# Optimization experiments

Measured on AMD Instinct MI355X. Metric: run time of the kernel, lower is better.

The kernel has to match this reference:

```python
import jax, jax.numpy as jnp
import numpy as np

D_MODEL, D_K, D_V, H, GRID = 512, 64, 64, 8, 196
B = 4


def setup_inputs() -> dict:
    key = jax.random.key(0)
    ks = jax.random.split(key, 12)
    s = 0.02
    return {
        "queries": jax.random.normal(ks[0], (B, GRID, D_MODEL), jnp.float32),
        "keys": jax.random.normal(ks[1], (B, GRID, D_MODEL), jnp.float32),
        "values": jax.random.normal(ks[2], (B, GRID, D_MODEL), jnp.float32),
        "Wq": jax.random.normal(ks[3], (H * D_K, D_MODEL), jnp.float32) * s,
        "bq": jnp.zeros((H * D_K,), jnp.float32),
        "Wk": jax.random.normal(ks[4], (H * D_K, D_MODEL), jnp.float32) * s,
        "bk": jnp.zeros((H * D_K,), jnp.float32),
        "Wv": jax.random.normal(ks[5], (H * D_V, D_MODEL), jnp.float32) * s,
        "bv": jnp.zeros((H * D_V,), jnp.float32),
        "Wo": jax.random.normal(ks[6], (D_MODEL, H * D_V), jnp.float32) * s,
        "bo": jnp.zeros((D_MODEL,), jnp.float32),
        "scale": jnp.ones((1, H, GRID, GRID), jnp.float32) / np.sqrt(D_K).astype(np.float32),
    }


def reference(queries, keys, values, Wq, bq, Wk, bk, Wv, bv, Wo, bo, scale):
    b, nq, _ = queries.shape
    nk = values.shape[1]
    # linear projections (torch nn.Linear: x @ W.T + b)
    q_sig = queries @ Wq.T + bq          # (b, nq, h*dk)
    k_p = keys @ Wk.T + bk               # (b, nk, h*dk)
    v_p = values @ Wv.T + bv             # (b, nk, h*dv)
    # elementwise q*k interaction (b, nq, nk, h*dk)
    att_e = q_sig[:, :, None, :] * k_p[:, None, :, :]
    # sigmoid-gated values
    v_g = jax.nn.sigmoid(att_e) * v_p[:, None, :, :]
    v = v_g.reshape(b, nq, nk, H, D_K).transpose(0, 3, 1, 2, 4)      # (b,h,nq,nk,dk)
    att = att_e.reshape(b, nq, nk, H, D_K).transpose(0, 3, 1, 2, 4)  # (b,h,nq,nk,dk)
    att = att.sum(-1) * scale            # (b,h,nq,nk)
    p = jax.nn.softmax(att, axis=-1)     # dropout is identity in eval mode
    # (att.unsqueeze(-2) @ v).squeeze(-2)
    image = jnp.einsum("bhqk,bhqkd->bhqd", p, v)
    image = image.transpose(0, 2, 1, 3).reshape(b, nq, H * D_V)
    out = image @ Wo.T + bo              # (b, nq, d_model)
    out = jax.nn.sigmoid(q_sig * out) * out
    return out
```

## Files before the change

kernel.cpp:

```cpp
#include <hip/hip_runtime.h>
#include <hip/hip_bf16.h>
#include <math.h>

#define NQ 196
#define BATCH 4
#define HD 512
#define NH 8
#define DK 64
#define MROWS 784
#define MPAD 832

typedef __attribute__((ext_vector_type(8))) short short8;
typedef __attribute__((ext_vector_type(4))) short short4v;
typedef __attribute__((ext_vector_type(4))) float float4v;

__device__ __forceinline__ float b2f(short s) {
  return __uint_as_float(((unsigned)(unsigned short)s) << 16);
}
__device__ __forceinline__ short f2b(float x) {
  return __builtin_bit_cast(short, __float2bfloat16(x));
}
__device__ __forceinline__ float fexp2(float x) {
  float r; asm("v_exp_f32 %0, %1" : "=v"(r) : "v"(x)); return r;
}
__device__ __forceinline__ float frcp(float x) {
  float r; asm("v_rcp_f32 %0, %1" : "=v"(r) : "v"(x)); return r;
}
__device__ __forceinline__ void cvt4(float4 v, short4v& hi, short4v& lo) {
  float x[4] = {v.x, v.y, v.z, v.w};
  #pragma unroll
  for (int i = 0; i < 4; ++i) {
    hi[i] = f2b(x[i]);
    lo[i] = f2b(x[i] - b2f(hi[i]));
  }
}

struct ProjArgs {
  const float* X[3]; const float* W[3]; const float* bias[3];
  float* Cf[3]; short* Ch[3]; short* Cl[3];
};

__global__ __launch_bounds__(256)
void proj_gemm(ProjArgs p, int M, int N, int K) {
  const int z = blockIdx.z;
  const float* __restrict__ X = p.X[z];
  const float* __restrict__ W = p.W[z];

  __shared__ short ldsA[2][2][32 * 32];
  __shared__ short ldsB[2][2][64 * 32];

  const int t = threadIdx.x;
  const int w = t >> 6, ln = t & 63;
  const int lm = ln & 15, quad = ln >> 4;
  const int m0 = blockIdx.x * 32, n0 = blockIdx.y * 64;

  const int aRow = t >> 3, aK = (t & 7) << 2;
  const int bRow = t >> 2, bK = (t & 3) << 3;
  const int ar = min(m0 + aRow, M - 1);
  const float* Ap = X + (size_t)ar * K + aK;
  const float* Bp = W + (size_t)(n0 + bRow) * K + bK;

  const int wm = (w & 1) << 4, wn = (w >> 1) << 5;
  float4v acc[2] = {{0.f,0.f,0.f,0.f},{0.f,0.f,0.f,0.f}};

  float4 ra  = *(const float4*)Ap;
  float4 rb0 = *(const float4*)Bp;
  float4 rb1 = *(const float4*)(Bp + 4);

  const int T = K >> 5;
  for (int kt = 0; kt < T; ++kt) {
    const int buf = kt & 1;
    short4v ahi, alo; cvt4(ra, ahi, alo);
    short4v bh0, bl0, bh1, bl1; cvt4(rb0, bh0, bl0); cvt4(rb1, bh1, bl1);
    *(short4v*)&ldsA[buf][0][aRow * 32 + aK] = ahi;
    *(short4v*)&ldsA[buf][1][aRow * 32 + aK] = alo;
    short8 bh = {bh0[0],bh0[1],bh0[2],bh0[3],bh1[0],bh1[1],bh1[2],bh1[3]};
    short8 bl = {bl0[0],bl0[1],bl0[2],bl0[3],bl1[0],bl1[1],bl1[2],bl1[3]};
    *(short8*)&ldsB[buf][0][bRow * 32 + bK] = bh;
    *(short8*)&ldsB[buf][1][bRow * 32 + bK] = bl;
    __syncthreads();
    if (kt + 1 < T) {
      ra  = *(const float4*)(Ap + (size_t)(kt + 1) * 32);
      rb0 = *(const float4*)(Bp + (size_t)(kt + 1) * 32);
      rb1 = *(const float4*)(Bp + (size_t)(kt + 1) * 32 + 4);
    }
    short8 fah = *(const short8*)&ldsA[buf][0][(wm + lm) * 32 + (quad << 3)];
    short8 fal = *(const short8*)&ldsA[buf][1][(wm + lm) * 32 + (quad << 3)];
    #pragma unroll
    for (int ni = 0; ni < 2; ++ni) {
      short8 fbh = *(const short8*)&ldsB[buf][0][(wn + (ni << 4) + lm) * 32 + (quad << 3)];
      short8 fbl = *(const short8*)&ldsB[buf][1][(wn + (ni << 4) + lm) * 32 + (quad << 3)];
      acc[ni] = __builtin_amdgcn_mfma_f32_16x16x32_bf16(fah, fbh, acc[ni], 0,0,0);
      acc[ni] = __builtin_amdgcn_mfma_f32_16x16x32_bf16(fah, fbl, acc[ni], 0,0,0);
      acc[ni] = __builtin_amdgcn_mfma_f32_16x16x32_bf16(fal, fbh, acc[ni], 0,0,0);
    }
  }

  const float* bias = p.bias[z];
  float* Cf = p.Cf[z]; short* Ch = p.Ch[z]; short* Cl = p.Cl[z];
  #pragma unroll
  for (int ni = 0; ni < 2; ++ni) {
    const int n = n0 + wn + (ni << 4) + lm;
    const float bv = bias[n];
    #pragma unroll
    for (int r = 0; r < 4; ++r) {
      const int m = m0 + wm + (quad << 2) + r;
      if (m < M) {
        const float c = acc[ni][r] + bv;
        if (Cf) Cf[(size_t)m * N + n] = c;
        if (Ch) {
          const short hi = f2b(c);
          Ch[(size_t)m * N + n] = hi;
          Cl[(size_t)m * N + n] = f2b(c - b2f(hi));
        }
      }
    }
  }
}

__global__ __launch_bounds__(256)
void out_gemm(const float* __restrict__ part, const float* __restrict__ W,
              const float* __restrict__ bias, const float* __restrict__ qsg,
              float* __restrict__ C, int M, int N, int K) {
  __shared__ short ldsA[2][2][32 * 32];
  __shared__ short ldsB[2][2][64 * 32];

  const int t = threadIdx.x;
  const int w = t >> 6, ln = t & 63;
  const int lm = ln & 15, quad = ln >> 4;
  const int m0 = blockIdx.x * 32, n0 = blockIdx.y * 64;

  const int aRow = t >> 3, aK = (t & 7) << 2;
  const int bRow = t >> 2, bK = (t & 3) << 3;
  const int ar = min(m0 + aRow, M - 1);
  const size_t NELF = (size_t)MROWS * HD;
  const float* Ap = part + (size_t)ar * K + aK;
  const float* Bp = W + (size_t)(n0 + bRow) * K + bK;

  const int wm = (w & 1) << 4, wn = (w >> 1) << 5;
  float4v acc[2] = {{0.f,0.f,0.f,0.f},{0.f,0.f,0.f,0.f}};

  float4 s0 = *(const float4*)(Ap);
  float4 s1 = *(const float4*)(Ap + NELF);
  float4 s2 = *(const float4*)(Ap + 2 * NELF);
  float4 s3 = *(const float4*)(Ap + 3 * NELF);
  float4 rb0 = *(const float4*)Bp;
  float4 rb1 = *(const float4*)(Bp + 4);

  const int T = K >> 5;
  for (int kt = 0; kt < T; ++kt) {
    const int buf = kt & 1;
    float4 ra = make_float4(s0.x+s1.x+s2.x+s3.x, s0.y+s1.y+s2.y+s3.y,
                            s0.z+s1.z+s2.z+s3.z, s0.w+s1.w+s2.w+s3.w);
    short4v ahi, alo; cvt4(ra, ahi, alo);
    short4v bh0, bl0, bh1, bl1; cvt4(rb0, bh0, bl0); cvt4(rb1, bh1, bl1);
    *(short4v*)&ldsA[buf][0][aRow * 32 + aK] = ahi;
    *(short4v*)&ldsA[buf][1][aRow * 32 + aK] = alo;
    short8 bh = {bh0[0],bh0[1],bh0[2],bh0[3],bh1[0],bh1[1],bh1[2],bh1[3]};
    short8 bl = {bl0[0],bl0[1],bl0[2],bl0[3],bl1[0],bl1[1],bl1[2],bl1[3]};
    *(short8*)&ldsB[buf][0][bRow * 32 + bK] = bh;
    *(short8*)&ldsB[buf][1][bRow * 32 + bK] = bl;
    __syncthreads();
    if (kt + 1 < T) {
      const size_t ko = (size_t)(kt + 1) * 32;
      s0 = *(const float4*)(Ap + ko);
      s1 = *(const float4*)(Ap + NELF + ko);
      s2 = *(const float4*)(Ap + 2 * NELF + ko);
      s3 = *(const float4*)(Ap + 3 * NELF + ko);
      rb0 = *(const float4*)(Bp + ko);
      rb1 = *(const float4*)(Bp + ko + 4);
    }
    short8 fah = *(const short8*)&ldsA[buf][0][(wm + lm) * 32 + (quad << 3)];
    short8 fal = *(const short8*)&ldsA[buf][1][(wm + lm) * 32 + (quad << 3)];
    #pragma unroll
    for (int ni = 0; ni < 2; ++ni) {
      short8 fbh = *(const short8*)&ldsB[buf][0][(wn + (ni << 4) + lm) * 32 + (quad << 3)];
      short8 fbl = *(const short8*)&ldsB[buf][1][(wn + (ni << 4) + lm) * 32 + (quad << 3)];
      acc[ni] = __builtin_amdgcn_mfma_f32_16x16x32_bf16(fah, fbh, acc[ni], 0,0,0);
      acc[ni] = __builtin_amdgcn_mfma_f32_16x16x32_bf16(fah, fbl, acc[ni], 0,0,0);
      acc[ni] = __builtin_amdgcn_mfma_f32_16x16x32_bf16(fal, fbh, acc[ni], 0,0,0);
    }
  }

  #pragma unroll
  for (int ni = 0; ni < 2; ++ni) {
    const int n = n0 + wn + (ni << 4) + lm;
    const float bv = bias[n];
    #pragma unroll
    for (int r = 0; r < 4; ++r) {
      const int m = m0 + wm + (quad << 2) + r;
      if (m < M) {
        float c = acc[ni][r] + bv;
        const float qg = qsg[(size_t)m * N + n];
        c = __fdividef(c, 1.f + __expf(-qg * c));
        C[(size_t)m * N + n] = c;
      }
    }
  }
}

__global__ __launch_bounds__(256)
void scores_softmax(const short* __restrict__ qsh, const short* __restrict__ qsl,
                    const short* __restrict__ ksh, const short* __restrict__ ksl,
                    const float* __restrict__ scg, float* __restrict__ pbuf) {
  const int q0 = blockIdx.x * 16;
  const int bh = blockIdx.y;
  const int b = bh >> 3, h = bh & 7;
  const int w = threadIdx.x >> 6, ln = threadIdx.x & 63;
  const int lm = ln & 15, quad = ln >> 4;
  const float L2E = 1.4426950408889634f;

  __shared__ float S[16][210];

  const size_t abase = ((size_t)(b * NQ) + q0 + lm) * HD + h * DK + (quad << 3);
  short8 ah0 = *(const short8*)(qsh + abase);
  short8 ah1 = *(const short8*)(qsh + abase + 32);
  short8 al0 = *(const short8*)(qsl + abase);
  short8 al1 = *(const short8*)(qsl + abase + 32);

  for (int nt = w; nt < 13; nt += 4) {
    const size_t bbase = ((size_t)(b * NQ) + nt * 16 + lm) * HD + h * DK + (quad << 3);
    short8 bh0 = *(const short8*)(ksh + bbase);
    short8 bh1 = *(const short8*)(ksh + bbase + 32);
    short8 bl0 = *(const short8*)(ksl + bbase);
    short8 bl1 = *(const short8*)(ksl + bbase + 32);
    float4v acc = {0.f, 0.f, 0.f, 0.f};
    acc = __builtin_amdgcn_mfma_f32_16x16x32_bf16(ah0, bh0, acc, 0,0,0);
    acc = __builtin_amdgcn_mfma_f32_16x16x32_bf16(ah1, bh1, acc, 0,0,0);
    acc = __builtin_amdgcn_mfma_f32_16x16x32_bf16(ah0, bl0, acc, 0,0,0);
    acc = __builtin_amdgcn_mfma_f32_16x16x32_bf16(ah1, bl1, acc, 0,0,0);
    acc = __builtin_amdgcn_mfma_f32_16x16x32_bf16(al0, bh0, acc, 0,0,0);
    acc = __builtin_amdgcn_mfma_f32_16x16x32_bf16(al1, bh1, acc, 0,0,0);
    #pragma unroll
    for (int r = 0; r < 4; ++r)
      S[(quad << 2) + r][nt * 16 + lm] = acc[r];
  }
  __syncthreads();

  for (int i = 0; i < 4; ++i) {
    const int rr = (w << 2) + i;
    const int q = q0 + rr;
    const bool qok = q < NQ;
    const float* srow = scg + ((size_t)h * NQ + (qok ? q : 0)) * NQ;
    float att[4];
    #pragma unroll
    for (int j = 0; j < 4; ++j) {
      const int c = ln + (j << 6);
      att[j] = -1e30f;
      if (c < NQ) att[j] = S[rr][c] * srow[c] * L2E;
    }
    float m = fmaxf(fmaxf(att[0], att[1]), fmaxf(att[2], att[3]));
    #pragma unroll
    for (int off = 32; off; off >>= 1) m = fmaxf(m, __shfl_xor(m, off, 64));
    float e[4], s = 0.f;
    #pragma unroll
    for (int j = 0; j < 4; ++j) { e[j] = fexp2(att[j] - m); s += e[j]; }
    #pragma unroll
    for (int off = 32; off; off >>= 1) s += __shfl_xor(s, off, 64);
    const float rinv = __fdividef(1.f, s);
    if (qok) {
      float* prow = pbuf + (((size_t)(b * NH + h) * NQ) + q) * NQ;
      #pragma unroll
      for (int j = 0; j < 4; ++j) {
        const int c = ln + (j << 6);
        if (c < NQ) prow[c] = e[j] * rinv;
      }
    }
  }
}

__global__ __launch_bounds__(512)
void pv_kernel(const float* __restrict__ qsg, const float* __restrict__ kpg,
               const float* __restrict__ vpg, const float* __restrict__ pbuf,
               float* __restrict__ part) {
  const int b  = blockIdx.y;
  const int x  = blockIdx.x;
  const int ks = x & 3;
  const int q0 = (x >> 2) << 2;
  const int hd = threadIdx.x;
  const int h  = hd >> 6;
  const float LOG2E = 1.4426950408889634f;

  const size_t r0 = ((size_t)(b * NQ) + q0) * HD + hd;
  float nqs[4];
  #pragma unroll
  for (int qi = 0; qi < 4; ++qi)
    nqs[qi] = -qsg[r0 + (size_t)qi * HD] * LOG2E;

  const float* kp = kpg + (size_t)b * NQ * HD + hd;
  const float* vp = vpg + (size_t)b * NQ * HD + hd;
  const float* pr = pbuf + ((size_t)(b * NH + h) * NQ + q0) * NQ;

  float acc[4] = {0.f, 0.f, 0.f, 0.f};
  const int kbeg = ks * 49;
  for (int k = kbeg; k < kbeg + 49; ++k) {
    const float kv = kp[(size_t)k * HD];
    const float vv = vp[(size_t)k * HD];
    #pragma unroll
    for (int qi = 0; qi < 4; ++qi) {
      const float e = fexp2(nqs[qi] * kv);
      const float g = vv * frcp(1.f + e);
      acc[qi] += pr[(size_t)qi * NQ + k] * g;
    }
  }
  float* dst = part + (size_t)ks * ((size_t)MROWS * HD) + r0;
  #pragma unroll
  for (int qi = 0; qi < 4; ++qi) dst[(size_t)qi * HD] = acc[qi];
}

extern "C" void kernel_launch(void* const* d_in, const int* in_sizes, int n_in,
                              void* d_out, int out_size, void* d_ws, size_t ws_size,
                              hipStream_t stream) {
  const float* queries = (const float*)d_in[0];
  const float* keys    = (const float*)d_in[1];
  const float* values  = (const float*)d_in[2];
  const float* Wq = (const float*)d_in[3];
  const float* bq = (const float*)d_in[4];
  const float* Wk = (const float*)d_in[5];
  const float* bk = (const float*)d_in[6];
  const float* Wv = (const float*)d_in[7];
  const float* bv = (const float*)d_in[8];
  const float* Wo = (const float*)d_in[9];
  const float* bo = (const float*)d_in[10];
  const float* scale = (const float*)d_in[11];

  char* base = (char*)d_ws;
  const size_t FB = sizeof(float);
  const size_t NELF  = (size_t)MROWS * HD;
  const size_t NELPS = (size_t)MPAD * HD;

  size_t o = 0;
  float* q_sig = (float*)(base + o); o += NELF * FB;
  float* k_p   = (float*)(base + o); o += NELF * FB;
  float* v_p   = (float*)(base + o); o += NELF * FB;
  float* pbuf  = (float*)(base + o); o += (size_t)BATCH * NH * NQ * NQ * FB;
  short* qsh = (short*)(base + o); o += NELPS * 2;
  short* qsl = (short*)(base + o); o += NELPS * 2;
  short* ksh = (short*)(base + o); o += NELPS * 2;
  short* ksl = (short*)(base + o); o += NELPS * 2;
  float* part = (float*)(base + o); o += 4 * NELF * FB;

  ProjArgs gp;
  gp.X[0] = queries; gp.W[0] = Wq; gp.bias[0] = bq;
  gp.Cf[0] = q_sig;  gp.Ch[0] = qsh; gp.Cl[0] = qsl;
  gp.X[1] = keys;    gp.W[1] = Wk; gp.bias[1] = bk;
  gp.Cf[1] = k_p;    gp.Ch[1] = ksh; gp.Cl[1] = ksl;
  gp.X[2] = values;  gp.W[2] = Wv; gp.bias[2] = bv;
  gp.Cf[2] = v_p;    gp.Ch[2] = nullptr; gp.Cl[2] = nullptr;
  proj_gemm<<<dim3(25, HD/64, 3), 256, 0, stream>>>(gp, MROWS, HD, HD);

  scores_softmax<<<dim3(13, NH*BATCH), 256, 0, stream>>>(qsh, qsl, ksh, ksl, scale, pbuf);

  pv_kernel<<<dim3(196, BATCH), 512, 0, stream>>>(q_sig, k_p, v_p, pbuf, part);

  out_gemm<<<dim3(25, HD/64, 1), 256, 0, stream>>>(part, Wo, bo, q_sig,
                                                   (float*)d_out, MROWS, HD, HD);
}
```

Before: 144.1 us.

## Pre-split weights to bf16 hi/lo, split-K GEMMs with async LDS loads, finer pv grid

Adds a kernel that converts all four weight matrices to bf16 hi/lo pairs once per call, so the GEMMs no longer redo that conversion per tile. The weights are then streamed straight into LDS with global_load_lds. Both GEMMs now run 512 threads as two K-halves and reduce the partial sums through shared memory, which doubles the waves per tile. pv_kernel is split over two head-dimension halves with 256-thread blocks to raise the block count. The cost is an extra launch, extra workspace traffic and the LDS reduction step.

```diff
diff --git a/kernel.cpp b/kernel.cpp
--- a/kernel.cpp
+++ b/kernel.cpp
@@ -34,132 +34,183 @@
     lo[i] = f2b(x[i] - b2f(hi[i]));
   }
 }
+__device__ __forceinline__ void gload_lds16(const void* g, void* l) {
+  __builtin_amdgcn_global_load_lds(
+      (const __attribute__((address_space(1))) unsigned int*)g,
+      (__attribute__((address_space(3))) unsigned int*)l, 16, 0, 0);
+}
+
+struct WSplitArgs { const float* src[4]; short* hi[4]; short* lo[4]; };
+
+__global__ __launch_bounds__(256)
+void wsplit_kernel(WSplitArgs a) {
+  const int seg = blockIdx.x >> 7;
+  const size_t off = (size_t)(blockIdx.x & 127) * 2048 + (size_t)threadIdx.x * 8;
+  const float* src = a.src[seg] + off;
+  float4 v0 = *(const float4*)(src);
+  float4 v1 = *(const float4*)(src + 4);
+  short4v h0, l0, h1, l1;
+  cvt4(v0, h0, l0); cvt4(v1, h1, l1);
+  short8 vh = {h0[0],h0[1],h0[2],h0[3],h1[0],h1[1],h1[2],h1[3]};
+  short8 vl = {l0[0],l0[1],l0[2],l0[3],l1[0],l1[1],l1[2],l1[3]};
+  *(short8*)(a.hi[seg] + off) = vh;
+  *(short8*)(a.lo[seg] + off) = vl;
+}
+
 
 struct ProjArgs {
-  const float* X[3]; const float* W[3]; const float* bias[3];
+  const float* X[3]; const short* Wh[3]; const short* Wl[3]; const float* bias[3];
   float* Cf[3]; short* Ch[3]; short* Cl[3];
 };
 
-__global__ __launch_bounds__(256)
+__global__ __launch_bounds__(512)
 void proj_gemm(ProjArgs p, int M, int N, int K) {
   const int z = blockIdx.z;
-  const float* __restrict__ X = p.X[z];
-  const float* __restrict__ W = p.W[z];
-
-  __shared__ short ldsA[2][2][32 * 32];
-  __shared__ short ldsB[2][2][64 * 32];
+  const float* __restrict__ X  = p.X[z];
+  const short* __restrict__ Wh = p.Wh[z];
+  const short* __restrict__ Wl = p.Wl[z];
+
+  __shared__ short smem[24576];
+  short* const A_ = smem;
+  short* const B_ = smem + 8192;
+  float* const redC = (float*)smem;
 
   const int t = threadIdx.x;
-  const int w = t >> 6, ln = t & 63;
-  const int lm = ln & 15, quad = ln >> 4;
+  const int g = t >> 8;
+  const int tt = t & 255;
+  const int ln = t & 63, lm = ln & 15, quad = ln >> 4;
+  const int w = (t >> 6) & 3;
   const int m0 = blockIdx.x * 32, n0 = blockIdx.y * 64;
-
-  const int aRow = t >> 3, aK = (t & 7) << 2;
-  const int bRow = t >> 2, bK = (t & 3) << 3;
+  const int kb = g << 8;
+
+  const int aRow = tt >> 3, aK = (tt & 7) << 2;
   const int ar = min(m0 + aRow, M - 1);
-  const float* Ap = X + (size_t)ar * K + aK;
-  const float* Bp = W + (size_t)(n0 + bRow) * K + bK;
+  const float* Ap = X + (size_t)ar * K + kb + aK;
+  const int aIdx = aRow * 32 + aK;
+  const int bRow = tt >> 2, bK = (tt & 3) << 3;
+  const short* Bph = Wh + (size_t)(n0 + bRow) * K + kb + bK;
+  const short* Bpl = Wl + (size_t)(n0 + bRow) * K + kb + bK;
 
   const int wm = (w & 1) << 4, wn = (w >> 1) << 5;
   float4v acc[2] = {{0.f,0.f,0.f,0.f},{0.f,0.f,0.f,0.f}};
 
-  float4 ra  = *(const float4*)Ap;
-  float4 rb0 = *(const float4*)Bp;
-  float4 rb1 = *(const float4*)(Bp + 4);
-
-  const int T = K >> 5;
+  const int T = 8;
+  float4 ra = *(const float4*)Ap;
+  gload_lds16(Bph, &B_[((g << 1) + 0) * 4096 + 0 * 2048 + tt * 8]);
+  gload_lds16(Bpl, &B_[((g << 1) + 0) * 4096 + 1 * 2048 + tt * 8]);
+  {
+    short4v ahi, alo; cvt4(ra, ahi, alo);
+    *(short4v*)&A_[((g << 1) + 0) * 2048 + 0 * 1024 + aIdx] = ahi;
+    *(short4v*)&A_[((g << 1) + 0) * 2048 + 1 * 1024 + aIdx] = alo;
+  }
+
   for (int kt = 0; kt < T; ++kt) {
     const int buf = kt & 1;
-    short4v ahi, alo; cvt4(ra, ahi, alo);
-    short4v bh0, bl0, bh1, bl1; cvt4(rb0, bh0, bl0); cvt4(rb1, bh1, bl1);
-    *(short4v*)&ldsA[buf][0][aRow * 32 + aK] = ahi;
-    *(short4v*)&ldsA[buf][1][aRow * 32 + aK] = alo;
-    short8 bh = {bh0[0],bh0[1],bh0[2],bh0[3],bh1[0],bh1[1],bh1[2],bh1[3]};
-    short8 bl = {bl0[0],bl0[1],bl0[2],bl0[3],bl1[0],bl1[1],bl1[2],bl1[3]};
-    *(short8*)&ldsB[buf][0][bRow * 32 + bK] = bh;
-    *(short8*)&ldsB[buf][1][bRow * 32 + bK] = bl;
     __syncthreads();
     if (kt + 1 < T) {
-      ra  = *(const float4*)(Ap + (size_t)(kt + 1) * 32);
-      rb0 = *(const float4*)(Bp + (size_t)(kt + 1) * 32);
-      rb1 = *(const float4*)(Bp + (size_t)(kt + 1) * 32 + 4);
-    }
-    short8 fah = *(const short8*)&ldsA[buf][0][(wm + lm) * 32 + (quad << 3)];
-    short8 fal = *(const short8*)&ldsA[buf][1][(wm + lm) * 32 + (quad << 3)];
+      ra = *(const float4*)(Ap + (size_t)(kt + 1) * 32);
+      const int nb = buf ^ 1;
+      gload_lds16(Bph + (size_t)(kt + 1) * 32, &B_[((g << 1) + nb) * 4096 + 0 * 2048 + tt * 8]);
+      gload_lds16(Bpl + (size_t)(kt + 1) * 32, &B_[((g << 1) + nb) * 4096 + 1 * 2048 + tt * 8]);
+    }
+    const short* Ab = &A_[((g << 1) + buf) * 2048];
+    const short* Bb = &B_[((g << 1) + buf) * 4096];
+    short8 fah = *(const short8*)&Ab[0 * 1024 + (wm + lm) * 32 + (quad << 3)];
+    short8 fal = *(const short8*)&Ab[1 * 1024 + (wm + lm) * 32 + (quad << 3)];
     #pragma unroll
     for (int ni = 0; ni < 2; ++ni) {
-      short8 fbh = *(const short8*)&ldsB[buf][0][(wn + (ni << 4) + lm) * 32 + (quad << 3)];
-      short8 fbl = *(const short8*)&ldsB[buf][1][(wn + (ni << 4) + lm) * 32 + (quad << 3)];
+      short8 fbh = *(const short8*)&Bb[0 * 2048 + (wn + (ni << 4) + lm) * 32 + (quad << 3)];
+      short8 fbl = *(const short8*)&Bb[1 * 2048 + (wn + (ni << 4) + lm) * 32 + (quad << 3)];
       acc[ni] = __builtin_amdgcn_mfma_f32_16x16x32_bf16(fah, fbh, acc[ni], 0,0,0);
       acc[ni] = __builtin_amdgcn_mfma_f32_16x16x32_bf16(fah, fbl, acc[ni], 0,0,0);
       acc[ni] = __builtin_amdgcn_mfma_f32_16x16x32_bf16(fal, fbh, acc[ni], 0,0,0);
     }
-  }
-
-  const float* bias = p.bias[z];
-  float* Cf = p.Cf[z]; short* Ch = p.Ch[z]; short* Cl = p.Cl[z];
-  #pragma unroll
-  for (int ni = 0; ni < 2; ++ni) {
-    const int n = n0 + wn + (ni << 4) + lm;
-    const float bv = bias[n];
-    #pragma unroll
-    for (int r = 0; r < 4; ++r) {
-      const int m = m0 + wm + (quad << 2) + r;
-      if (m < M) {
-        const float c = acc[ni][r] + bv;
-        if (Cf) Cf[(size_t)m * N + n] = c;
-        if (Ch) {
-          const short hi = f2b(c);
-          Ch[(size_t)m * N + n] = hi;
-          Cl[(size_t)m * N + n] = f2b(c - b2f(hi));
+    if (kt + 1 < T) {
+      const int nb = buf ^ 1;
+      short4v ahi, alo; cvt4(ra, ahi, alo);
+      *(short4v*)&A_[((g << 1) + nb) * 2048 + 0 * 1024 + aIdx] = ahi;
+      *(short4v*)&A_[((g << 1) + nb) * 2048 + 1 * 1024 + aIdx] = alo;
+    }
+  }
+
+  __syncthreads();
+  if (g == 1) {
+    #pragma unroll
+    for (int ni = 0; ni < 2; ++ni)
+      *(float4v*)&redC[tt * 8 + ni * 4] = acc[ni];
+  }
+  __syncthreads();
+  if (g == 0) {
+    const float* bias = p.bias[z];
+    float* Cf = p.Cf[z]; short* Ch = p.Ch[z]; short* Cl = p.Cl[z];
+    #pragma unroll
+    for (int ni = 0; ni < 2; ++ni) {
+      const int n = n0 + wn + (ni << 4) + lm;
+      const float bv = bias[n];
+      #pragma unroll
+      for (int r = 0; r < 4; ++r) {
+        const int m = m0 + wm + (quad << 2) + r;
+        if (m < M) {
+          const float c = acc[ni][r] + redC[tt * 8 + ni * 4 + r] + bv;
+          if (Cf) Cf[(size_t)m * N + n] = c;
+          if (Ch) {
+            const short hi = f2b(c);
+            Ch[(size_t)m * N + n] = hi;
+            Cl[(size_t)m * N + n] = f2b(c - b2f(hi));
+          }
         }
       }
     }
   }
 }
 
-__global__ __launch_bounds__(256)
-void out_gemm(const float* __restrict__ part, const float* __restrict__ W,
-              const float* __restrict__ bias, const float* __restrict__ qsg,
-              float* __restrict__ C, int M, int N, int K) {
-  __shared__ short ldsA[2][2][32 * 32];
-  __shared__ short ldsB[2][2][64 * 32];
+__global__ __launch_bounds__(512)
+void out_gemm(const float* __restrict__ part, const short* __restrict__ Wh,
+              const short* __restrict__ Wl, const float* __restrict__ bias,
+              const float* __restrict__ qsg, float* __restrict__ C,
+              int M, int N, int K) {
+  __shared__ short smem[24576];
+  short* const A_ = smem;
+  short* const B_ = smem + 8192;
+  float* const redC = (float*)smem;
 
   const int t = threadIdx.x;
-  const int w = t >> 6, ln = t & 63;
-  const int lm = ln & 15, quad = ln >> 4;
+  const int g = t >> 8;
+  const int tt = t & 255;
+  const int ln = t & 63, lm = ln & 15, quad = ln >> 4;
+  const int w = (t >> 6) & 3;
   const int m0 = blockIdx.x * 32, n0 = blockIdx.y * 64;
-
-  const int aRow = t >> 3, aK = (t & 7) << 2;
-  const int bRow = t >> 2, bK = (t & 3) << 3;
+  const int kb = g << 8;
+  const size_t NELF = (size_t)MROWS * HD;
+
+  const int aRow = tt >> 3, aK = (tt & 7) << 2;
   const int ar = min(m0 + aRow, M - 1);
-  const size_t NELF = (size_t)MROWS * HD;
-  const float* Ap = part + (size_t)ar * K + aK;
-  const float* Bp = W + (size_t)(n0 + bRow) * K + bK;
+  const float* Ap = part + (size_t)ar * K + kb + aK;
+  const int aIdx = aRow * 32 + aK;
+  const int bRow = tt >> 2, bK = (tt & 3) << 3;
+  const short* Bph = Wh + (size_t)(n0 + bRow) * K + kb + bK;
+  const short* Bpl = Wl + (size_t)(n0 + bRow) * K + kb + bK;
 
   const int wm = (w & 1) << 4, wn = (w >> 1) << 5;
   float4v acc[2] = {{0.f,0.f,0.f,0.f},{0.f,0.f,0.f,0.f}};
 
+  const int T = 8;
   float4 s0 = *(const float4*)(Ap);
   float4 s1 = *(const float4*)(Ap + NELF);
   float4 s2 = *(const float4*)(Ap + 2 * NELF);
   float4 s3 = *(const float4*)(Ap + 3 * NELF);
-  float4 rb0 = *(const float4*)Bp;
-  float4 rb1 = *(const float4*)(Bp + 4);
-
-  const int T = K >> 5;
-  for (int kt = 0; kt < T; ++kt) {
-    const int buf = kt & 1;
+  gload_lds16(Bph, &B_[((g << 1) + 0) * 4096 + 0 * 2048 + tt * 8]);
+  gload_lds16(Bpl, &B_[((g << 1) + 0) * 4096 + 1 * 2048 + tt * 8]);
+  {
     float4 ra = make_float4(s0.x+s1.x+s2.x+s3.x, s0.y+s1.y+s2.y+s3.y,
                             s0.z+s1.z+s2.z+s3.z, s0.w+s1.w+s2.w+s3.w);
     short4v ahi, alo; cvt4(ra, ahi, alo);
-    short4v bh0, bl0, bh1, bl1; cvt4(rb0, bh0, bl0); cvt4(rb1, bh1, bl1);
-    *(short4v*)&ldsA[buf][0][aRow * 32 + aK] = ahi;
-    *(short4v*)&ldsA[buf][1][aRow * 32 + aK] = alo;
-    short8 bh = {bh0[0],bh0[1],bh0[2],bh0[3],bh1[0],bh1[1],bh1[2],bh1[3]};
-    short8 bl = {bl0[0],bl0[1],bl0[2],bl0[3],bl1[0],bl1[1],bl1[2],bl1[3]};
-    *(short8*)&ldsB[buf][0][bRow * 32 + bK] = bh;
-    *(short8*)&ldsB[buf][1][bRow * 32 + bK] = bl;
+    *(short4v*)&A_[((g << 1) + 0) * 2048 + 0 * 1024 + aIdx] = ahi;
+    *(short4v*)&A_[((g << 1) + 0) * 2048 + 1 * 1024 + aIdx] = alo;
+  }
+
+  for (int kt = 0; kt < T; ++kt) {
+    const int buf = kt & 1;
     __syncthreads();
     if (kt + 1 < T) {
       const size_t ko = (size_t)(kt + 1) * 32;
@@ -167,33 +218,53 @@
       s1 = *(const float4*)(Ap + NELF + ko);
       s2 = *(const float4*)(Ap + 2 * NELF + ko);
       s3 = *(const float4*)(Ap + 3 * NELF + ko);
-      rb0 = *(const float4*)(Bp + ko);
-      rb1 = *(const float4*)(Bp + ko + 4);
-    }
-    short8 fah = *(const short8*)&ldsA[buf][0][(wm + lm) * 32 + (quad << 3)];
-    short8 fal = *(const short8*)&ldsA[buf][1][(wm + lm) * 32 + (quad << 3)];
+      const int nb = buf ^ 1;
+      gload_lds16(Bph + ko, &B_[((g << 1) + nb) * 4096 + 0 * 2048 + tt * 8]);
+      gload_lds16(Bpl + ko, &B_[((g << 1) + nb) * 4096 + 1 * 2048 + tt * 8]);
+    }
+    const short* Ab = &A_[((g << 1) + buf) * 2048];
+    const short* Bb = &B_[((g << 1) + buf) * 4096];
+    short8 fah = *(const short8*)&Ab[0 * 1024 + (wm + lm) * 32 + (quad << 3)];
+    short8 fal = *(const short8*)&Ab[1 * 1024 + (wm + lm) * 32 + (quad << 3)];
     #pragma unroll
     for (int ni = 0; ni < 2; ++ni) {
-      short8 fbh = *(const short8*)&ldsB[buf][0][(wn + (ni << 4) + lm) * 32 + (quad << 3)];
-      short8 fbl = *(const short8*)&ldsB[buf][1][(wn + (ni << 4) + lm) * 32 + (quad << 3)];
+      short8 fbh = *(const short8*)&Bb[0 * 2048 + (wn + (ni << 4) + lm) * 32 + (quad << 3)];
+      short8 fbl = *(const short8*)&Bb[1 * 2048 + (wn + (ni << 4) + lm) * 32 + (quad << 3)];
       acc[ni] = __builtin_amdgcn_mfma_f32_16x16x32_bf16(fah, fbh, acc[ni], 0,0,0);
       acc[ni] = __builtin_amdgcn_mfma_f32_16x16x32_bf16(fah, fbl, acc[ni], 0,0,0);
       acc[ni] = __builtin_amdgcn_mfma_f32_16x16x32_bf16(fal, fbh, acc[ni], 0,0,0);
     }
-  }
-
-  #pragma unroll
-  for (int ni = 0; ni < 2; ++ni) {
-    const int n = n0 + wn + (ni << 4) + lm;
-    const float bv = bias[n];
-    #pragma unroll
-    for (int r = 0; r < 4; ++r) {
-      const int m = m0 + wm + (quad << 2) + r;
-      if (m < M) {
-        float c = acc[ni][r] + bv;
-        const float qg = qsg[(size_t)m * N + n];
-        c = __fdividef(c, 1.f + __expf(-qg * c));
-        C[(size_t)m * N + n] = c;
+    if (kt + 1 < T) {
+      const int nb = buf ^ 1;
+      float4 ra = make_float4(s0.x+s1.x+s2.x+s3.x, s0.y+s1.y+s2.y+s3.y,
+                              s0.z+s1.z+s2.z+s3.z, s0.w+s1.w+s2.w+s3.w);
+      short4v ahi, alo; cvt4(ra, ahi, alo);
+      *(short4v*)&A_[((g << 1) + nb) * 2048 + 0 * 1024 + aIdx] = ahi;
+      *(short4v*)&A_[((g << 1) + nb) * 2048 + 1 * 1024 + aIdx] = alo;
+    }
+  }
+
+  __syncthreads();
+  if (g == 1) {
+    #pragma unroll
+    for (int ni = 0; ni < 2; ++ni)
+      *(float4v*)&redC[tt * 8 + ni * 4] = acc[ni];
+  }
+  __syncthreads();
+  if (g == 0) {
+    #pragma unroll
+    for (int ni = 0; ni < 2; ++ni) {
+      const int n = n0 + wn + (ni << 4) + lm;
+      const float bv = bias[n];
+      #pragma unroll
+      for (int r = 0; r < 4; ++r) {
+        const int m = m0 + wm + (quad << 2) + r;
+        if (m < M) {
+          float c = acc[ni][r] + redC[tt * 8 + ni * 4 + r] + bv;
+          const float qg = qsg[(size_t)m * N + n];
+          c = __fdividef(c, 1.f + __expf(-qg * c));
+          C[(size_t)m * N + n] = c;
+        }
       }
     }
   }
@@ -269,15 +340,17 @@
   }
 }
 
-__global__ __launch_bounds__(512)
+__global__ __launch_bounds__(256)
 void pv_kernel(const float* __restrict__ qsg, const float* __restrict__ kpg,
                const float* __restrict__ vpg, const float* __restrict__ pbuf,
                float* __restrict__ part) {
   const int b  = blockIdx.y;
   const int x  = blockIdx.x;
-  const int ks = x & 3;
-  const int q0 = (x >> 2) << 2;
-  const int hd = threadIdx.x;
+  const int qg = x >> 3;
+  const int ks = (x >> 1) & 3;
+  const int dh = x & 1;
+  const int q0 = qg << 2;
+  const int hd = (dh << 8) + threadIdx.x;
   const int h  = hd >> 6;
   const float LOG2E = 1.4426950408889634f;
 
@@ -328,6 +401,7 @@
   const size_t FB = sizeof(float);
   const size_t NELF  = (size_t)MROWS * HD;
   const size_t NELPS = (size_t)MPAD * HD;
+  const size_t WEL   = (size_t)HD * HD;
 
   size_t o = 0;
   float* q_sig = (float*)(base + o); o += NELF * FB;
@@ -338,21 +412,36 @@
   short* qsl = (short*)(base + o); o += NELPS * 2;
   short* ksh = (short*)(base + o); o += NELPS * 2;
   short* ksl = (short*)(base + o); o += NELPS * 2;
+  short* Wqh = (short*)(base + o); o += WEL * 2;
+  short* Wql = (short*)(base + o); o += WEL * 2;
+  short* Wkh = (short*)(base + o); o += WEL * 2;
+  short* Wkl = (short*)(base + o); o += WEL * 2;
+  short* Wvh = (short*)(base + o); o += WEL * 2;
+  short* Wvl = (short*)(base + o); o += WEL * 2;
+  short* Woh = (short*)(base + o); o += WEL * 2;
+  short* Wol = (short*)(base + o); o += WEL * 2;
   float* part = (float*)(base + o); o += 4 * NELF * FB;
 
+  WSplitArgs wa;
+  wa.src[0] = Wq; wa.hi[0] = Wqh; wa.lo[0] = Wql;
+  wa.src[1] = Wk; wa.hi[1] = Wkh; wa.lo[1] = Wkl;
+  wa.src[2] = Wv; wa.hi[2] = Wvh; wa.lo[2] = Wvl;
+  wa.src[3] = Wo; wa.hi[3] = Woh; wa.lo[3] = Wol;
+  wsplit_kernel<<<512, 256, 0, stream>>>(wa);
+
   ProjArgs gp;
-  gp.X[0] = queries; gp.W[0] = Wq; gp.bias[0] = bq;
+  gp.X[0] = queries; gp.Wh[0] = Wqh; gp.Wl[0] = Wql; gp.bias[0] = bq;
   gp.Cf[0] = q_sig;  gp.Ch[0] = qsh; gp.Cl[0] = qsl;
-  gp.X[1] = keys;    gp.W[1] = Wk; gp.bias[1] = bk;
+  gp.X[1] = keys;    gp.Wh[1] = Wkh; gp.Wl[1] = Wkl; gp.bias[1] = bk;
   gp.Cf[1] = k_p;    gp.Ch[1] = ksh; gp.Cl[1] = ksl;
-  gp.X[2] = values;  gp.W[2] = Wv; gp.bias[2] = bv;
+  gp.X[2] = values;  gp.Wh[2] = Wvh; gp.Wl[2] = Wvl; gp.bias[2] = bv;
   gp.Cf[2] = v_p;    gp.Ch[2] = nullptr; gp.Cl[2] = nullptr;
-  proj_gemm<<<dim3(25, HD/64, 3), 256, 0, stream>>>(gp, MROWS, HD, HD);
+  proj_gemm<<<dim3(25, HD/64, 3), 512, 0, stream>>>(gp, MROWS, HD, HD);
 
   scores_softmax<<<dim3(13, NH*BATCH), 256, 0, stream>>>(qsh, qsl, ksh, ksl, scale, pbuf);
 
-  pv_kernel<<<dim3(196, BATCH), 512, 0, stream>>>(q_sig, k_p, v_p, pbuf, part);
-
-  out_gemm<<<dim3(25, HD/64, 1), 256, 0, stream>>>(part, Wo, bo, q_sig,
-                                                   (float*)d_out, MROWS, HD, HD);
-}
+  pv_kernel<<<dim3(392, BATCH), 256, 0, stream>>>(q_sig, k_p, v_p, pbuf, part);
+
+  out_gemm<<<dim3(25, HD/64), 512, 0, stream>>>(part, Woh, Wol, bo, q_sig,
+                                                (float*)d_out, MROWS, HD, HD);
+}
```

After: 145.2 us. Within noise of the previous version (+0.7%).
